# Kernel tuning notes

Hardware: AMD Instinct MI355X
Metric: run time of the kernel (lower is better)

## Reference

```python
import jax, jax.numpy as jnp
import numpy as np

MAX_VAL = 10000.0
KS = (1, 5, 10, 20, 50)
B, V, L = 256, 128000, 200


def setup_inputs() -> dict:
    key = jax.random.key(0)
    k1, k2, k3 = jax.random.split(key, 3)
    scores = jax.random.normal(k1, (B, V), dtype=jnp.float32)
    labels = jax.random.randint(k2, (B,), 0, V, dtype=jnp.int64)
    seqs = jax.random.randint(k3, (B, L), 0, V, dtype=jnp.int64)
    return {"scores": scores, "labels": labels, "seqs": seqs}


def reference(scores, labels, seqs):
    b = scores.shape[0]
    rows = jnp.arange(b)
    # gather predicted score for the true label BEFORE masking (torch order)
    predicts = scores[rows, labels]  # [B]
    # scatter -MAX_VAL at history items (masked scatter)
    masked = scores.at[rows[:, None], seqs].set(-MAX_VAL)  # [B, V]
    valid_length = (masked > -MAX_VAL).sum(-1).astype(jnp.float32)  # [B]
    rank = (predicts[:, None] < masked).sum(-1).astype(jnp.float32)  # [B]
    res = []
    for k in KS:
        indicator = (rank < k).astype(jnp.float32)
        res.append((indicator / jnp.log2(rank + 2.0)).mean())  # NDCG@k
        res.append(indicator.mean())  # Recall@k
    res.append((1.0 / (rank + 1.0)).mean())  # MRR
    res.append((1.0 - rank / valid_length).mean())  # AUC-like
    res.append(jnp.float32(0.0))
    return jnp.stack(res)
```

## Files before the change

### kernel.cpp

```cpp
#include <hip/hip_runtime.h>
#include <math.h>

#define B_CONST 256
#define V_CONST 128000
#define L_CONST 200
#define SLICES  25

typedef float f32x4 __attribute__((ext_vector_type(4)));


__global__ __launch_bounds__(256) void rank_count_kernel(
    const float* __restrict__ scores,
    const int* __restrict__ labels,
    const int* __restrict__ seqs,
    int* __restrict__ partial,
    int* __restrict__ sub,
    int* __restrict__ dist)
{
    const int slice = blockIdx.x;
    const int b     = blockIdx.y;
    const int tid   = threadIdx.x;
    const int wave  = tid >> 6;

    const float* row = scores + (size_t)b * V_CONST;

    const f32x4* row4 = (const f32x4*)row;
    const int base = slice * 1280 + tid;
    f32x4 a0 = __builtin_nontemporal_load(row4 + base);
    f32x4 a1 = __builtin_nontemporal_load(row4 + base + 256);
    f32x4 a2 = __builtin_nontemporal_load(row4 + base + 512);
    f32x4 a3 = __builtin_nontemporal_load(row4 + base + 768);
    f32x4 a4 = __builtin_nontemporal_load(row4 + base + 1024);

    const float predict = row[labels[b]];

    __shared__ int s_seq[L_CONST];
    __shared__ int s_wcnt[4];
    __shared__ int s_wsub[4];
    __shared__ int s_wdist[4];

    int myseq = 0;
    float sv = 0.0f;
    if (slice == 0 && tid < L_CONST) {
        myseq = seqs[b * L_CONST + tid];
        s_seq[tid] = myseq;
        sv = row[myseq];
    }

    int cnt = 0;
    cnt += (a0[0] > predict) + (a0[1] > predict) + (a0[2] > predict) + (a0[3] > predict);
    cnt += (a1[0] > predict) + (a1[1] > predict) + (a1[2] > predict) + (a1[3] > predict);
    cnt += (a2[0] > predict) + (a2[1] > predict) + (a2[2] > predict) + (a2[3] > predict);
    cnt += (a3[0] > predict) + (a3[1] > predict) + (a3[2] > predict) + (a3[3] > predict);
    cnt += (a4[0] > predict) + (a4[1] > predict) + (a4[2] > predict) + (a4[3] > predict);

    #pragma unroll
    for (int off = 32; off > 0; off >>= 1)
        cnt += __shfl_down(cnt, off, 64);
    if ((tid & 63) == 0) s_wcnt[wave] = cnt;

    __syncthreads();

    if (slice == 0) {
        int idist = 0, isub = 0;
        if (tid < L_CONST) {
            bool first = true;
            for (int j = 0; j < tid; ++j) {
                if (s_seq[j] == myseq) { first = false; break; }
            }
            if (first) {
                idist = 1;
                if (sv > predict) isub = 1;
            }
        }
        #pragma unroll
        for (int off = 32; off > 0; off >>= 1) {
            idist += __shfl_down(idist, off, 64);
            isub  += __shfl_down(isub,  off, 64);
        }
        if ((tid & 63) == 0) { s_wsub[wave] = isub; s_wdist[wave] = idist; }
        __syncthreads();
        if (tid == 0) {
            sub[b]  = s_wsub[0] + s_wsub[1] + s_wsub[2] + s_wsub[3];
            dist[b] = s_wdist[0] + s_wdist[1] + s_wdist[2] + s_wdist[3];
        }
    }

    if (tid == 0)
        partial[slice * B_CONST + b] = s_wcnt[0] + s_wcnt[1] + s_wcnt[2] + s_wcnt[3];
}

__global__ __launch_bounds__(64) void finalize_kernel(
    const int* __restrict__ partial,
    const int* __restrict__ sub,
    const int* __restrict__ dist,
    float* __restrict__ out)
{
    const int l = threadIdx.x;

    float acc[12];
    #pragma unroll
    for (int q = 0; q < 12; ++q) acc[q] = 0.0f;

    const float ks[5] = {1.0f, 5.0f, 10.0f, 20.0f, 50.0f};

    #pragma unroll
    for (int r = 0; r < 4; ++r) {
        const int b = l + 64 * r;
        int gt = 0;
        #pragma unroll
        for (int s = 0; s < SLICES; ++s) gt += partial[s * B_CONST + b];
        const float rank  = (float)(gt - sub[b]);
        const float valid = (float)(V_CONST - dist[b]);

        const float invlog = 1.0f / log2f(rank + 2.0f);
        #pragma unroll
        for (int i = 0; i < 5; ++i) {
            const float ind = (rank < ks[i]) ? 1.0f : 0.0f;
            acc[2 * i]     += ind * invlog;
            acc[2 * i + 1] += ind;
        }
        acc[10] += 1.0f / (rank + 1.0f);
        acc[11] += 1.0f - rank / valid;
    }

    #pragma unroll
    for (int q = 0; q < 12; ++q) {
        float v = acc[q];
        #pragma unroll
        for (int off = 32; off > 0; off >>= 1)
            v += __shfl_down(v, off, 64);
        if (l == 0) out[q] = v * (1.0f / B_CONST);
    }
    if (l == 0) out[12] = 0.0f;
}

extern "C" void kernel_launch(void* const* d_in, const int* in_sizes, int n_in,
                              void* d_out, int out_size, void* d_ws, size_t ws_size,
                              hipStream_t stream) {
    const float* scores = (const float*)d_in[0];
    const int*   labels = (const int*)d_in[1];
    const int*   seqs   = (const int*)d_in[2];
    float* out = (float*)d_out;
    int*   ws  = (int*)d_ws;

    int* partial = ws;
    int* sub     = ws + SLICES * B_CONST;
    int* dist    = ws + SLICES * B_CONST + B_CONST;

    rank_count_kernel<<<dim3(SLICES, B_CONST), 256, 0, stream>>>(
        scores, labels, seqs, partial, sub, dist);
    finalize_kernel<<<1, 64, 0, stream>>>(partial, sub, dist, out);
}
```

Before: 198.1 us.

## Give each wave a slice, dedicate a wave to history dedup, use ballot counts

Each row's work is reorganised so that every 64-lane wave independently handles one 1280-float4 slice with 20 loads in flight per lane. A separate 26th wave per row deduplicates the history items using shuffles instead of shared memory, which removes __syncthreads and the serial O(L) scan that slice-0 blocks previously ran. Counting switches to ballot plus popcount, and blocks shrink to 128 threads with a 13xB grid. This removes block-level synchronisation and the dedup critical path from the streaming waves, at the cost of higher register pressure from 20 vector loads per lane and an O(L) shuffle loop in the dedup wave.

```diff
diff --git a/kernel.cpp b/kernel.cpp
--- a/kernel.cpp
+++ b/kernel.cpp
@@ -5,11 +5,13 @@
 #define V_CONST 128000
 #define L_CONST 200
 #define SLICES  25
+#define F4_PER_SLICE 1280
+#define F4_PER_LANE  20
 
 typedef float f32x4 __attribute__((ext_vector_type(4)));
 
 
-__global__ __launch_bounds__(256) void rank_count_kernel(
+__global__ __launch_bounds__(128, 4) void rank_count_kernel(
     const float* __restrict__ scores,
     const int* __restrict__ labels,
     const int* __restrict__ seqs,
@@ -17,77 +19,61 @@
     int* __restrict__ sub,
     int* __restrict__ dist)
 {
-    const int slice = blockIdx.x;
-    const int b     = blockIdx.y;
-    const int tid   = threadIdx.x;
-    const int wave  = tid >> 6;
+    const int lane = threadIdx.x & 63;
+    const int b    = blockIdx.y;
+    const int t    = blockIdx.x * 2 + (threadIdx.x >> 6);
 
     const float* row = scores + (size_t)b * V_CONST;
 
-    const f32x4* row4 = (const f32x4*)row;
-    const int base = slice * 1280 + tid;
-    f32x4 a0 = __builtin_nontemporal_load(row4 + base);
-    f32x4 a1 = __builtin_nontemporal_load(row4 + base + 256);
-    f32x4 a2 = __builtin_nontemporal_load(row4 + base + 512);
-    f32x4 a3 = __builtin_nontemporal_load(row4 + base + 768);
-    f32x4 a4 = __builtin_nontemporal_load(row4 + base + 1024);
-
     const float predict = row[labels[b]];
 
-    __shared__ int s_seq[L_CONST];
-    __shared__ int s_wcnt[4];
-    __shared__ int s_wsub[4];
-    __shared__ int s_wdist[4];
+    if (t < SLICES) {
+        const f32x4* row4 = (const f32x4*)row;
+        const int base = t * F4_PER_SLICE + lane;
+        f32x4 v[F4_PER_LANE];
+        #pragma unroll
+        for (int k = 0; k < F4_PER_LANE; ++k)
+            v[k] = __builtin_nontemporal_load(row4 + base + k * 64);
 
-    int myseq = 0;
-    float sv = 0.0f;
-    if (slice == 0 && tid < L_CONST) {
-        myseq = seqs[b * L_CONST + tid];
-        s_seq[tid] = myseq;
-        sv = row[myseq];
-    }
-
-    int cnt = 0;
-    cnt += (a0[0] > predict) + (a0[1] > predict) + (a0[2] > predict) + (a0[3] > predict);
-    cnt += (a1[0] > predict) + (a1[1] > predict) + (a1[2] > predict) + (a1[3] > predict);
-    cnt += (a2[0] > predict) + (a2[1] > predict) + (a2[2] > predict) + (a2[3] > predict);
-    cnt += (a3[0] > predict) + (a3[1] > predict) + (a3[2] > predict) + (a3[3] > predict);
-    cnt += (a4[0] > predict) + (a4[1] > predict) + (a4[2] > predict) + (a4[3] > predict);
-
-    #pragma unroll
-    for (int off = 32; off > 0; off >>= 1)
-        cnt += __shfl_down(cnt, off, 64);
-    if ((tid & 63) == 0) s_wcnt[wave] = cnt;
-
-    __syncthreads();
-
-    if (slice == 0) {
-        int idist = 0, isub = 0;
-        if (tid < L_CONST) {
-            bool first = true;
-            for (int j = 0; j < tid; ++j) {
-                if (s_seq[j] == myseq) { first = false; break; }
-            }
-            if (first) {
-                idist = 1;
-                if (sv > predict) isub = 1;
+        int cnt = 0;
+        #pragma unroll
+        for (int k = 0; k < F4_PER_LANE; ++k) {
+            cnt += __popcll(__ballot(v[k][0] > predict));
+            cnt += __popcll(__ballot(v[k][1] > predict));
+            cnt += __popcll(__ballot(v[k][2] > predict));
+            cnt += __popcll(__ballot(v[k][3] > predict));
+        }
+        if (lane == 0) partial[t * B_CONST + b] = cnt;
+    } else {
+        const int* sq = seqs + b * L_CONST;
+        int e[4], val[4];
+        float sv[4];
+        #pragma unroll
+        for (int k = 0; k < 4; ++k) {
+            e[k]   = lane + 64 * k;
+            val[k] = (e[k] < L_CONST) ? sq[e[k]] : -1;
+            sv[k]  = (e[k] < L_CONST) ? row[val[k]] : -1.0e30f;
+        }
+        bool first[4] = {true, true, true, true};
+        #pragma unroll
+        for (int jb = 0; jb < 4; ++jb) {
+            for (int l = 0; l < 64; ++l) {
+                const int j  = jb * 64 + l;
+                const int sj = __shfl(val[jb], l);
+                #pragma unroll
+                for (int k = jb; k < 4; ++k)
+                    if (j < e[k] && sj == val[k]) first[k] = false;
             }
         }
+        int d = 0, s = 0;
         #pragma unroll
-        for (int off = 32; off > 0; off >>= 1) {
-            idist += __shfl_down(idist, off, 64);
-            isub  += __shfl_down(isub,  off, 64);
+        for (int k = 0; k < 4; ++k) {
+            const bool isdist = first[k] && (e[k] < L_CONST);
+            d += __popcll(__ballot(isdist));
+            s += __popcll(__ballot(isdist && (sv[k] > predict)));
         }
-        if ((tid & 63) == 0) { s_wsub[wave] = isub; s_wdist[wave] = idist; }
-        __syncthreads();
-        if (tid == 0) {
-            sub[b]  = s_wsub[0] + s_wsub[1] + s_wsub[2] + s_wsub[3];
-            dist[b] = s_wdist[0] + s_wdist[1] + s_wdist[2] + s_wdist[3];
-        }
+        if (lane == 0) { dist[b] = d; sub[b] = s; }
     }
-
-    if (tid == 0)
-        partial[slice * B_CONST + b] = s_wcnt[0] + s_wcnt[1] + s_wcnt[2] + s_wcnt[3];
 }
 
 __global__ __launch_bounds__(64) void finalize_kernel(
@@ -148,7 +134,7 @@
     int* sub     = ws + SLICES * B_CONST;
     int* dist    = ws + SLICES * B_CONST + B_CONST;
 
-    rank_count_kernel<<<dim3(SLICES, B_CONST), 256, 0, stream>>>(
+    rank_count_kernel<<<dim3(13, B_CONST), 128, 0, stream>>>(
         scores, labels, seqs, partial, sub, dist);
     finalize_kernel<<<1, 64, 0, stream>>>(partial, sub, dist, out);
 }
```

Result: no change. 195.9 us (-1.1%).
